# Performance work log

Hardware: AMD Instinct MI355X
Metric: run time of the kernel (lower is better)

The kernel has to match this reference:

```python
import jax, jax.numpy as jnp
import numpy as np

B, S, HID = 2, 2048, 2048
NH, HD, RD = 16, 128, 64
KVC, QC = 512, 1536


def _apply_rope(t):
    # t: [B, H, S, R]; standard half-split rotary embedding
    R = t.shape[-1]
    s = t.shape[-2]
    inv_freq = 1.0 / (10000.0 ** (jnp.arange(0, R, 2, dtype=jnp.float32) / R))  # [R/2]
    ang = jnp.arange(s, dtype=jnp.float32)[:, None] * inv_freq[None, :]  # [S, R/2]
    cos, sin = jnp.cos(ang), jnp.sin(ang)
    t1, t2 = t[..., : R // 2], t[..., R // 2 :]
    return jnp.concatenate([t1 * cos - t2 * sin, t2 * cos + t1 * sin], axis=-1)


def setup_inputs() -> dict:
    key = jax.random.key(0)
    ks = jax.random.split(key, 20)

    def lin(k, fan_in, fan_out):
        bound = 1.0 / np.sqrt(fan_in)
        kw, kb = jax.random.split(k)
        W = jax.random.uniform(kw, (fan_in, fan_out), jnp.float32, -bound, bound)
        b = jax.random.uniform(kb, (fan_out,), jnp.float32, -bound, bound)
        return W, b

    x = jax.random.normal(ks[0], (B, S, HID), jnp.float32)
    W_kvd, b_kvd = lin(ks[1], HID, KVC)
    W_ku, b_ku = lin(ks[2], KVC, NH * HD)
    W_vu, b_vu = lin(ks[3], KVC, NH * HD)
    W_kr, b_kr = lin(ks[4], KVC, NH * RD)
    W_qd, b_qd = lin(ks[5], HID, QC)
    W_qu, b_qu = lin(ks[6], QC, NH * HD)
    W_qr, b_qr = lin(ks[7], QC, NH * RD)
    W_o, b_o = lin(ks[8], NH * HD, HID)
    return dict(x=x, W_kvd=W_kvd, b_kvd=b_kvd, W_ku=W_ku, b_ku=b_ku,
                W_vu=W_vu, b_vu=b_vu, W_kr=W_kr, b_kr=b_kr,
                W_qd=W_qd, b_qd=b_qd, W_qu=W_qu, b_qu=b_qu,
                W_qr=W_qr, b_qr=b_qr, W_o=W_o, b_o=b_o)


def reference(x, W_kvd, b_kvd, W_ku, b_ku, W_vu, b_vu, W_kr, b_kr,
              W_qd, b_qd, W_qu, b_qu, W_qr, b_qr, W_o, b_o):
    b, s, _ = x.shape

    def heads(t, d):  # [B,S,NH*d] -> [B,NH,S,d]
        return t.reshape(b, s, NH, d).transpose(0, 2, 1, 3)

    kv_c = x @ W_kvd + b_kvd                     # [B,S,KVC]
    keys_c = heads(kv_c @ W_ku + b_ku, HD)       # [B,H,S,HD]
    values = heads(kv_c @ W_vu + b_vu, HD)
    keys_r = _apply_rope(heads(kv_c @ W_kr + b_kr, RD))

    q_c = x @ W_qd + b_qd                        # [B,S,QC]
    queries_c = heads(q_c @ W_qu + b_qu, HD)
    queries_r = _apply_rope(heads(q_c @ W_qr + b_qr, RD))

    q = jnp.concatenate([queries_c, queries_r], axis=-1)  # [B,H,S,HD+RD]
    k = jnp.concatenate([keys_c, keys_r], axis=-1)

    scale = 1.0 / np.sqrt(HD + RD)
    scores = jnp.einsum('bhqd,bhkd->bhqk', q, k) * scale
    causal = jnp.triu(jnp.ones((s, s), dtype=bool), k=1)
    scores = jnp.where(causal[None, None], jnp.float32(-1e9), scores)
    probs = jax.nn.softmax(scores, axis=-1)
    ctx = jnp.einsum('bhqk,bhkd->bhqd', probs, values)    # [B,H,S,HD]
    ctx = ctx.transpose(0, 2, 1, 3).reshape(b, s, NH * HD)
    return ctx @ W_o + b_o
```

## Files before the change

### kernel.cpp

```cpp
#include <hip/hip_runtime.h>
#include <math.h>

#define BB   2
#define SS   2048
#define HIDD 2048
#define NHH  16
#define HDD  128
#define RDD  64
#define KVCC 512
#define QCC  1536
#define DQK  192
#define MROWS 4096

using bf16x8 = __attribute__((ext_vector_type(8))) short;
using short4v = __attribute__((ext_vector_type(4))) short;
using f32x4  = __attribute__((ext_vector_type(4))) float;
using f32x16 = __attribute__((ext_vector_type(16))) float;

static __device__ __forceinline__ float b2f(short s) {
    unsigned u = ((unsigned)(unsigned short)s) << 16;
    union { unsigned u; float f; } v; v.u = u; return v.f;
}
static __device__ __forceinline__ short f2b(float f) {
    union { float f; unsigned u; } v; v.f = f;
    unsigned r = (v.u + 0x7fffu + ((v.u >> 16) & 1u)) >> 16;
    return (short)r;
}
static __device__ __forceinline__ unsigned cvtpk(float lo, float hi) {
    unsigned r;
    asm("v_cvt_pk_bf16_f32 %0, %1, %2" : "=v"(r) : "v"(lo), "v"(hi));
    return r;
}

#define GLOAD16(gsrc, ldst) \
    __builtin_amdgcn_global_load_lds((const __attribute__((address_space(1))) void*)(gsrc), \
                                     (__attribute__((address_space(3))) void*)(ldst), 16, 0, 0)

__global__ void prep_kernel(
    const float* __restrict__ W0, const float* __restrict__ W1,
    const float* __restrict__ W2, const float* __restrict__ W3,
    const float* __restrict__ W4, const float* __restrict__ W5,
    const float* __restrict__ W6, const float* __restrict__ W7,
    short* __restrict__ D0, short* __restrict__ D1,
    short* __restrict__ D2, short* __restrict__ D3,
    const float* __restrict__ x, short* __restrict__ xb,
    float2* __restrict__ tab) {
    __shared__ float t[32][33];
    int bid = blockIdx.x;
    int tx = threadIdx.x, ty = threadIdx.y;
    if (bid >= 17408) {
        int entry = (bid - 17408) * 256 + ty * 32 + tx;
        int s = entry >> 5, i = entry & 31;
        float inv = exp2f(-(float)i * 0.41524101186092034f);
        float sn, cs;
        sincosf((float)s * inv, &sn, &cs);
        tab[entry] = make_float2(cs, sn);
        return;
    }
    if (bid >= 15360) {
        int base = (bid - 15360) * 4096 + (ty * 32 + tx) * 16;
#pragma unroll
        for (int c = 0; c < 4; c++) {
            float4 v = *(const float4*)(x + base + c * 4);
            short4v o;
            o[0] = f2b(v.x); o[1] = f2b(v.y); o[2] = f2b(v.z); o[3] = f2b(v.w);
            *(short4v*)(xb + base + c * 4) = o;
        }
        return;
    }
    const float* W; short* Dst; int K, N, lt;
    if (bid < 4096) {
        if (bid < 1024) { W = W0; Dst = D0;                        K = 2048; N = 512;  lt = bid; }
        else            { W = W1; Dst = D0 + (size_t)512 * 2048;   K = 2048; N = 1536; lt = bid - 1024; }
    } else if (bid < 6656) {
        if (bid < 5120)      { W = W2; Dst = D1;                       K = 512; N = 2048; lt = bid - 4096; }
        else if (bid < 6144) { W = W3; Dst = D1 + (size_t)2048 * 512;  K = 512; N = 2048; lt = bid - 5120; }
        else                 { W = W4; Dst = D1 + (size_t)4096 * 512;  K = 512; N = 1024; lt = bid - 6144; }
    } else if (bid < 11264) {
        if (bid < 9728) { W = W5; Dst = D2;                        K = 1536; N = 2048; lt = bid - 6656; }
        else            { W = W6; Dst = D2 + (size_t)2048 * 1536;  K = 1536; N = 1024; lt = bid - 9728; }
    } else { W = W7; Dst = D3; K = 2048; N = 2048; lt = bid - 11264; }
    int ntx = N >> 5;
    int n0 = (lt % ntx) * 32, k0 = (lt / ntx) * 32;
#pragma unroll
    for (int i = 0; i < 4; i++)
        t[ty + i * 8][tx] = W[(size_t)(k0 + ty + i * 8) * N + n0 + tx];
    __syncthreads();
#pragma unroll
    for (int i = 0; i < 4; i++)
        Dst[(size_t)(n0 + ty + i * 8) * K + k0 + tx] = f2b(t[tx][ty + i * 8]);
}

template <int ID>
__global__ __launch_bounds__(256) void gemm128(
    const short* __restrict__ A, const short* __restrict__ Bt,
    const float* __restrict__ b0, const float* __restrict__ b1, const float* __restrict__ b2,
    void* __restrict__ C0, void* __restrict__ C1,
    const float2* __restrict__ tab,
    int M, int N, int K) {
    __shared__ short Asm[3][4096];
    __shared__ short Bsm[3][4096];
    int tid = threadIdx.x, lane = tid & 63, w = tid >> 6;
    int wm = w >> 1, wn = w & 1;
    int nbx = N >> 7;
    int cpx = gridDim.x >> 3;
    int swz = ((int)blockIdx.x & 7) * cpx + ((int)blockIdx.x >> 3);
    int m0 = (swz / nbx) * 128, n0 = (swz % nbx) * 128;
    int fr = lane & 15, fk = (lane >> 4) * 8;
    const short* Ag = A + (size_t)(m0 + (tid >> 2)) * K + (tid & 3) * 8;
    const short* Bg = Bt + (size_t)(n0 + (tid >> 2)) * K + (tid & 3) * 8;
    auto stage = [&](int t, int b) {
        int k0 = t * 32;
        GLOAD16(Ag + k0, &Asm[b][tid * 8]);
        GLOAD16(Ag + k0 + (size_t)64 * K, &Asm[b][2048 + tid * 8]);
        GLOAD16(Bg + k0, &Bsm[b][tid * 8]);
        GLOAD16(Bg + k0 + (size_t)64 * K, &Bsm[b][2048 + tid * 8]);
    };
    f32x4 acc[4][4] = {};
    int NT = K >> 5;
    stage(0, 0);
    stage(1, 1);
    for (int t = 0; t < NT; t++) {
        int cur = t % 3;
        if (t + 1 < NT) asm volatile("s_waitcnt vmcnt(4)" ::: "memory");
        else            asm volatile("s_waitcnt vmcnt(0)" ::: "memory");
        __builtin_amdgcn_s_barrier();
        bf16x8 af[4], bfv[4];
#pragma unroll
        for (int m = 0; m < 4; m++)
            af[m] = *(const bf16x8*)&Asm[cur][(wm * 64 + m * 16 + fr) * 32 + fk];
#pragma unroll
        for (int n = 0; n < 4; n++)
            bfv[n] = *(const bf16x8*)&Bsm[cur][(wn * 64 + n * 16 + fr) * 32 + fk];
#pragma unroll
        for (int m = 0; m < 4; m++)
#pragma unroll
            for (int n = 0; n < 4; n++)
                acc[m][n] = __builtin_amdgcn_mfma_f32_16x16x32_bf16(af[m], bfv[n], acc[m][n], 0, 0, 0);
        __builtin_amdgcn_s_barrier();
        if (t + 2 < NT) stage(t + 2, (t + 2) % 3);
    }
    bool ropeTile = (ID == 2 && n0 >= 4096) || (ID == 3 && n0 >= 2048);
    if (ropeTile) {
        int cbase = n0 - (ID == 2 ? 4096 : 2048) + wn * 64;
        int h = cbase >> 6;
        const float* bias = (ID == 2) ? b2 : b1;
        short* Dst = (short*)C0;
#pragma unroll
        for (int m = 0; m < 4; m++)
#pragma unroll
            for (int r = 0; r < 4; r++) {
                int row = m0 + wm * 64 + m * 16 + ((lane >> 4) << 2) + r;
                int b = row >> 11, s = row & (SS - 1);
                short* o = Dst + (((size_t)(b * NHH + h)) * SS + s) * DQK + HDD + (cbase & 63);
#pragma unroll
                for (int pp = 0; pp < 2; pp++) {
                    int i = pp * 16 + fr;
                    float2 cs = tab[s * 32 + i];
                    float vlo = acc[m][pp][r] + bias[cbase + pp * 16 + fr];
                    float vhi = acc[m][pp + 2][r] + bias[cbase + pp * 16 + 32 + fr];
                    o[i] = f2b(vlo * cs.x - vhi * cs.y);
                    o[i + 32] = f2b(vhi * cs.x + vlo * cs.y);
                }
            }
        return;
    }
#pragma unroll
    for (int m = 0; m < 4; m++)
#pragma unroll
        for (int n = 0; n < 4; n++)
#pragma unroll
            for (int r = 0; r < 4; r++) {
                int row = m0 + wm * 64 + m * 16 + ((lane >> 4) << 2) + r;
                int col = n0 + wn * 64 + n * 16 + fr;
                float v = acc[m][n][r];
                if constexpr (ID == 0) {
                    ((float*)C0)[(size_t)row * N + col] = v + b0[col];
                } else if constexpr (ID == 1) {
                    if (col < KVCC)
                        ((short*)C0)[(size_t)row * KVCC + col] = f2b(v + b0[col]);
                    else
                        ((short*)C1)[(size_t)row * QCC + (col - KVCC)] = f2b(v + b1[col - KVCC]);
                } else if constexpr (ID == 2) {
                    int b = row >> 11, s = row & (SS - 1);
                    if (col < 2048) {
                        int h = col >> 7, d = col & 127;
                        ((short*)C0)[(((size_t)(b * NHH + h)) * SS + s) * DQK + d] = f2b(v + b0[col]);
                    } else {
                        int c = col - 2048; int h = c >> 7, d = c & 127;
                        ((short*)C1)[(((size_t)(b * NHH + h)) * HDD + d) * SS + s] = f2b(v + b1[c]);
                    }
                } else {
                    int b = row >> 11, s = row & (SS - 1);
                    int h = col >> 7, d = col & 127;
                    ((short*)C0)[(((size_t)(b * NHH + h)) * SS + s) * DQK + d] = f2b(v + b0[col]);
                }
            }
}

__global__ __launch_bounds__(256, 2) void attn_kernel(
    const short* __restrict__ Q, const short* __restrict__ Kg,
    const short* __restrict__ Vt, short* __restrict__ ctx) {
    __shared__ short Ksm[2][64 * 192];
    __shared__ short Vsm[2][128 * 64];
    int tid = threadIdx.x, lane = tid & 63, w = tid >> 6;
    int hf = lane >> 5, l31 = lane & 31;
    int bid = blockIdx.x;
    int half = bid >> 8, a = (bid & 255) >> 5;
    int qt = half ? a : 15 - a;
    int bh = bid & 31;
    int bb = bh >> 4, hd = bh & 15;
    int q0 = qt * 128;
    const short* Qp = Q + (size_t)bh * SS * DQK;
    const short* Kp = Kg + (size_t)bh * SS * DQK;
    const char*  Vp = (const char*)(Vt + (size_t)bh * HDD * SS);
    int wr0 = q0 + w * 32;
    int qrow = wr0 + l31;
    const float scale = 0.07216878364870323f;
    const float L2E = 1.44269504088896f;

    bf16x8 qf[12];
#pragma unroll
    for (int s = 0; s < 12; s++)
        qf[s] = *(const bf16x8*)(Qp + (size_t)qrow * DQK + s * 16 + hf * 8);

    f32x16 acc[4] = {};
    float mrow = -1e30f, lsum = 0.f;
    int nt = 2 * qt + 2;

    auto stageK = [&](int key0, int b) {
#pragma unroll
        for (int pp = 0; pp < 6; pp++) {
            int flat = pp * 4096 + tid * 16;
            int row = flat / 384, bir = flat - row * 384;
            const char* src = (const char*)Kp + (size_t)(key0 + row) * 384 + (bir ^ ((row & 7) << 4));
            GLOAD16(src, (char*)Ksm[b] + flat);
        }
    };
    auto stageV = [&](int key0, int b) {
#pragma unroll
        for (int c = 0; c < 4; c++) {
            int flat = c * 4096 + tid * 16;
            int d = flat >> 7, bik = flat & 127;
            const char* src = Vp + (size_t)d * (SS * 2) + (size_t)key0 * 2 + (bik ^ ((d & 7) << 4));
            GLOAD16(src, (char*)Vsm[b] + flat);
        }
    };

    stageK(0, 0); stageV(0, 0);
    __syncthreads();

    for (int t0 = 0; t0 < nt; t0++) {
        int key0 = t0 * 64;
        int cur = t0 & 1;
        if (t0 + 1 < nt) { stageK(key0 + 64, cur ^ 1); stageV(key0 + 64, cur ^ 1); }
        bool active = (key0 <= wr0 + 31);
        if (active) {
            f32x16 z = {};
            f32x16 s0a = z, s0b = z, s1a = z, s1b = z;
            int xr = (l31 & 7) << 4;
            const char* Kb = (const char*)Ksm[cur];
            __builtin_amdgcn_s_setprio(1);
#pragma unroll
            for (int s = 0; s < 12; s += 2) {
                bf16x8 k0 = *(const bf16x8*)(Kb + l31 * 384 + ((s * 32 + hf * 16) ^ xr));
                bf16x8 k1 = *(const bf16x8*)(Kb + (32 + l31) * 384 + ((s * 32 + hf * 16) ^ xr));
                s0a = __builtin_amdgcn_mfma_f32_32x32x16_bf16(k0, qf[s], s0a, 0, 0, 0);
                s1a = __builtin_amdgcn_mfma_f32_32x32x16_bf16(k1, qf[s], s1a, 0, 0, 0);
                bf16x8 k0b = *(const bf16x8*)(Kb + l31 * 384 + (((s + 1) * 32 + hf * 16) ^ xr));
                bf16x8 k1b = *(const bf16x8*)(Kb + (32 + l31) * 384 + (((s + 1) * 32 + hf * 16) ^ xr));
                s0b = __builtin_amdgcn_mfma_f32_32x32x16_bf16(k0b, qf[s + 1], s0b, 0, 0, 0);
                s1b = __builtin_amdgcn_mfma_f32_32x32x16_bf16(k1b, qf[s + 1], s1b, 0, 0, 0);
            }
            __builtin_amdgcn_s_setprio(0);
            f32x16 sv0 = s0a + s0b, sv1 = s1a + s1b;
            bool domask = (key0 + 63 > wr0);
            float p[32];
#pragma unroll
            for (int t = 0; t < 2; t++)
#pragma unroll
                for (int r = 0; r < 16; r++) {
                    float v = (t ? sv1[r] : sv0[r]);
                    int key = key0 + 32 * t + (r & 3) + 8 * (r >> 2) + 4 * hf;
                    if (domask && key > qrow) v = -1e30f;
                    p[t * 16 + r] = v;
                }
            float tm[16];
#pragma unroll
            for (int i = 0; i < 16; i++) tm[i] = fmaxf(p[i], p[i + 16]);
#pragma unroll
            for (int i = 0; i < 8; i++) tm[i] = fmaxf(tm[i], tm[i + 8]);
#pragma unroll
            for (int i = 0; i < 4; i++) tm[i] = fmaxf(tm[i], tm[i + 4]);
            float pmaxs = fmaxf(fmaxf(tm[0], tm[1]), fmaxf(tm[2], tm[3])) * scale;
            if (__any(pmaxs > mrow + 8.f)) {
                float pc = fmaxf(pmaxs, __shfl_xor(pmaxs, 32, 64));
                float mn = fmaxf(mrow, pc);
                float al = exp2f((mrow - mn) * L2E);
                mrow = mn;
                lsum *= al;
                float arl[16];
#pragma unroll
                for (int r = 0; r < 16; r++)
                    arl[r] = __shfl(al, (r & 3) + 8 * (r >> 2) + 4 * hf, 64);
#pragma unroll
                for (int n = 0; n < 4; n++)
#pragma unroll
                    for (int r = 0; r < 16; r++)
                        acc[n][r] *= arl[r];
            }
            float sL = scale * L2E, mL = mrow * L2E;
#pragma unroll
            for (int i = 0; i < 32; i++)
                p[i] = exp2f(fmaf(p[i], sL, -mL));
            float ts[16];
#pragma unroll
            for (int i = 0; i < 16; i++) ts[i] = p[i] + p[i + 16];
#pragma unroll
            for (int i = 0; i < 8; i++) ts[i] = ts[i] + ts[i + 8];
#pragma unroll
            for (int i = 0; i < 4; i++) ts[i] = ts[i] + ts[i + 4];
            lsum += (ts[0] + ts[1]) + (ts[2] + ts[3]);
            bf16x8 afv[4];
#pragma unroll
            for (int g = 0; g < 4; g++) {
                int base = (g >> 1) * 16 + (g & 1) * 8;
                unsigned a01 = cvtpk(p[base + 0], p[base + 1]);
                unsigned a23 = cvtpk(p[base + 2], p[base + 3]);
                unsigned b01 = cvtpk(p[base + 4], p[base + 5]);
                unsigned b23 = cvtpk(p[base + 6], p[base + 7]);
                unsigned s0 = hf ? a01 : b01, s1 = hf ? a23 : b23;
                unsigned r0 = (unsigned)__shfl_xor((int)s0, 32, 64);
                unsigned r1 = (unsigned)__shfl_xor((int)s1, 32, 64);
                union { unsigned u[4]; bf16x8 v; } af;
                af.u[0] = hf ? r0 : a01;
                af.u[1] = hf ? r1 : a23;
                af.u[2] = hf ? b01 : r0;
                af.u[3] = hf ? b23 : r1;
                afv[g] = af.v;
            }
            const char* Vb = (const char*)Vsm[cur];
            __builtin_amdgcn_s_setprio(1);
#pragma unroll
            for (int g = 0; g < 4; g++)
#pragma unroll
                for (int n = 0; n < 4; n++) {
                    int d = n * 32 + l31;
                    bf16x8 vf = *(const bf16x8*)(Vb + d * 128 + ((g * 32 + hf * 16) ^ ((d & 7) << 4)));
                    acc[n] = __builtin_amdgcn_mfma_f32_32x32x16_bf16(afv[g], vf, acc[n], 0, 0, 0);
                }
            __builtin_amdgcn_s_setprio(0);
        }
        __syncthreads();
    }
    lsum += __shfl_xor(lsum, 32, 64);
    float rc = 1.0f / lsum;
    float rcl[16];
#pragma unroll
    for (int r = 0; r < 16; r++)
        rcl[r] = __shfl(rc, (r & 3) + 8 * (r >> 2) + 4 * hf, 64);
#pragma unroll
    for (int n = 0; n < 4; n++)
#pragma unroll
        for (int r = 0; r < 16; r++) {
            int row = wr0 + (r & 3) + 8 * (r >> 2) + 4 * hf;
            int d = n * 32 + l31;
            ctx[((size_t)(bb * SS + row)) * (NHH * HDD) + hd * HDD + d] = f2b(acc[n][r] * rcl[r]);
        }
}

extern "C" void kernel_launch(void* const* d_in, const int* in_sizes, int n_in,
                              void* d_out, int out_size, void* d_ws, size_t ws_size,
                              hipStream_t stream) {
    const float* x     = (const float*)d_in[0];
    const float* W_kvd = (const float*)d_in[1];  const float* b_kvd = (const float*)d_in[2];
    const float* W_ku  = (const float*)d_in[3];  const float* b_ku  = (const float*)d_in[4];
    const float* W_vu  = (const float*)d_in[5];  const float* b_vu  = (const float*)d_in[6];
    const float* W_kr  = (const float*)d_in[7];  const float* b_kr  = (const float*)d_in[8];
    const float* W_qd  = (const float*)d_in[9];  const float* b_qd  = (const float*)d_in[10];
    const float* W_qu  = (const float*)d_in[11]; const float* b_qu  = (const float*)d_in[12];
    const float* W_qr  = (const float*)d_in[13]; const float* b_qr  = (const float*)d_in[14];
    const float* W_o   = (const float*)d_in[15]; const float* b_o   = (const float*)d_in[16];
    float* out = (float*)d_out;

    char* p = (char*)d_ws;
    auto alloc = [&](size_t elems) {
        short* r = (short*)p;
        p += ((elems * 2) + 255) & ~(size_t)255;
        return r;
    };
    short* xb   = alloc((size_t)MROWS * HIDD);
    short* kvc  = alloc((size_t)MROWS * KVCC);
    short* qc   = alloc((size_t)MROWS * QCC);
    short* kbuf = alloc((size_t)BB * NHH * SS * DQK);
    short* qbuf = alloc((size_t)BB * NHH * SS * DQK);
    short* vtb  = alloc((size_t)BB * NHH * HDD * SS);
    short* ctx  = alloc((size_t)MROWS * NHH * HDD);
    short* Wt1  = alloc((size_t)2048 * 2048);
    short* Wt2  = alloc((size_t)5120 * 512);
    short* Wt3  = alloc((size_t)3072 * 1536);
    short* Wt4  = alloc((size_t)2048 * 2048);
    float2* tab = (float2*)alloc((size_t)65536 * 4);

    dim3 tb(32, 8);
    prep_kernel<<<dim3(17664), tb, 0, stream>>>(
        W_kvd, W_qd, W_ku, W_vu, W_kr, W_qu, W_qr, W_o, Wt1, Wt2, Wt3, Wt4,
        x, xb, tab);

    gemm128<1><<<dim3(512), 256, 0, stream>>>(
        xb, Wt1, b_kvd, b_qd, nullptr, kvc, qc, nullptr, MROWS, 2048, 2048);
    gemm128<2><<<dim3(1280), 256, 0, stream>>>(
        kvc, Wt2, b_ku, b_vu, b_kr, kbuf, vtb, tab, MROWS, 5120, 512);
    gemm128<3><<<dim3(768), 256, 0, stream>>>(
        qc, Wt3, b_qu, b_qr, nullptr, qbuf, nullptr, tab, MROWS, 3072, 1536);

    attn_kernel<<<dim3(512), 256, 0, stream>>>(qbuf, kbuf, vtb, ctx);

    gemm128<0><<<dim3(512), 256, 0, stream>>>(
        ctx, Wt4, b_o, nullptr, nullptr, out, nullptr, nullptr, MROWS, HIDD, NHH * HDD);
}
```

Measured before the change: 359.3 us.

## Software-pipeline QK of next tile with softmax/PV of current tile

Restructures the flash-attention key loop so the QK^T MFMAs for tile u are issued alongside the softmax and PV work for tile u-1. K and V staging are split into separately timed async loads, with fine-grained vmcnt waits and raw barriers replacing the full __syncthreads. The goal is to hide softmax latency behind matrix work and overlap the global-to-LDS loads. In exchange it holds more live score registers, and the correctness of the hand-written vmcnt counts depends on how many loads are in flight.

```diff
diff --git a/kernel.cpp b/kernel.cpp
--- a/kernel.cpp
+++ b/kernel.cpp
@@ -246,113 +246,138 @@
             GLOAD16(src, (char*)Vsm[b] + flat);
         }
     };
+    auto qk = [&](int u, const short* Kbuf, f32x16& o0, f32x16& o1) {
+        int key0 = u * 64;
+        if (key0 > wr0 + 31) return;
+        const char* Kb = (const char*)Kbuf;
+        f32x16 z = {};
+        f32x16 a0 = z, a1 = z;
+        int xr = (l31 & 7) << 4;
+        __builtin_amdgcn_s_setprio(1);
+#pragma unroll
+        for (int s = 0; s < 12; s++) {
+            bf16x8 k0 = *(const bf16x8*)(Kb + l31 * 384 + ((s * 32 + hf * 16) ^ xr));
+            bf16x8 k1 = *(const bf16x8*)(Kb + (32 + l31) * 384 + ((s * 32 + hf * 16) ^ xr));
+            a0 = __builtin_amdgcn_mfma_f32_32x32x16_bf16(k0, qf[s], a0, 0, 0, 0);
+            a1 = __builtin_amdgcn_mfma_f32_32x32x16_bf16(k1, qf[s], a1, 0, 0, 0);
+        }
+        __builtin_amdgcn_s_setprio(0);
+        o0 = a0; o1 = a1;
+    };
+    auto smpv = [&](int u, const f32x16& sv0, const f32x16& sv1, const short* Vbuf) {
+        int key0 = u * 64;
+        if (key0 > wr0 + 31) return;
+        bool domask = (key0 + 63 > wr0);
+        float p[32];
+#pragma unroll
+        for (int t = 0; t < 2; t++)
+#pragma unroll
+            for (int r = 0; r < 16; r++) {
+                float v = (t ? sv1[r] : sv0[r]);
+                int key = key0 + 32 * t + (r & 3) + 8 * (r >> 2) + 4 * hf;
+                if (domask && key > qrow) v = -1e30f;
+                p[t * 16 + r] = v;
+            }
+        float tm[16];
+#pragma unroll
+        for (int i = 0; i < 16; i++) tm[i] = fmaxf(p[i], p[i + 16]);
+#pragma unroll
+        for (int i = 0; i < 8; i++) tm[i] = fmaxf(tm[i], tm[i + 8]);
+#pragma unroll
+        for (int i = 0; i < 4; i++) tm[i] = fmaxf(tm[i], tm[i + 4]);
+        float pmaxs = fmaxf(fmaxf(tm[0], tm[1]), fmaxf(tm[2], tm[3])) * scale;
+        if (__any(pmaxs > mrow + 8.f)) {
+            float pc = fmaxf(pmaxs, __shfl_xor(pmaxs, 32, 64));
+            float mn = fmaxf(mrow, pc);
+            float al = exp2f((mrow - mn) * L2E);
+            mrow = mn;
+            lsum *= al;
+            float arl[16];
+#pragma unroll
+            for (int r = 0; r < 16; r++)
+                arl[r] = __shfl(al, (r & 3) + 8 * (r >> 2) + 4 * hf, 64);
+#pragma unroll
+            for (int n = 0; n < 4; n++)
+#pragma unroll
+                for (int r = 0; r < 16; r++)
+                    acc[n][r] *= arl[r];
+        }
+        float sL = scale * L2E, mL = mrow * L2E;
+#pragma unroll
+        for (int i = 0; i < 32; i++)
+            p[i] = exp2f(fmaf(p[i], sL, -mL));
+        float ts[16];
+#pragma unroll
+        for (int i = 0; i < 16; i++) ts[i] = p[i] + p[i + 16];
+#pragma unroll
+        for (int i = 0; i < 8; i++) ts[i] = ts[i] + ts[i + 8];
+#pragma unroll
+        for (int i = 0; i < 4; i++) ts[i] = ts[i] + ts[i + 4];
+        lsum += (ts[0] + ts[1]) + (ts[2] + ts[3]);
+        bf16x8 afv[4];
+#pragma unroll
+        for (int g = 0; g < 4; g++) {
+            int base = (g >> 1) * 16 + (g & 1) * 8;
+            unsigned a01 = cvtpk(p[base + 0], p[base + 1]);
+            unsigned a23 = cvtpk(p[base + 2], p[base + 3]);
+            unsigned b01 = cvtpk(p[base + 4], p[base + 5]);
+            unsigned b23 = cvtpk(p[base + 6], p[base + 7]);
+            unsigned s0 = hf ? a01 : b01, s1 = hf ? a23 : b23;
+            unsigned r0 = (unsigned)__shfl_xor((int)s0, 32, 64);
+            unsigned r1 = (unsigned)__shfl_xor((int)s1, 32, 64);
+            union { unsigned u[4]; bf16x8 v; } af;
+            af.u[0] = hf ? r0 : a01;
+            af.u[1] = hf ? r1 : a23;
+            af.u[2] = hf ? b01 : r0;
+            af.u[3] = hf ? b23 : r1;
+            afv[g] = af.v;
+        }
+        const char* Vb = (const char*)Vbuf;
+        __builtin_amdgcn_s_setprio(1);
+#pragma unroll
+        for (int g = 0; g < 4; g++)
+#pragma unroll
+            for (int n = 0; n < 4; n++) {
+                int d = n * 32 + l31;
+                bf16x8 vf = *(const bf16x8*)(Vb + d * 128 + ((g * 32 + hf * 16) ^ ((d & 7) << 4)));
+                acc[n] = __builtin_amdgcn_mfma_f32_32x32x16_bf16(afv[g], vf, acc[n], 0, 0, 0);
+            }
+        __builtin_amdgcn_s_setprio(0);
+    };
+
+    f32x16 svA0 = {}, svA1 = {}, svB0 = {}, svB1 = {};
 
     stageK(0, 0); stageV(0, 0);
-    __syncthreads();
-
-    for (int t0 = 0; t0 < nt; t0++) {
-        int key0 = t0 * 64;
-        int cur = t0 & 1;
-        if (t0 + 1 < nt) { stageK(key0 + 64, cur ^ 1); stageV(key0 + 64, cur ^ 1); }
-        bool active = (key0 <= wr0 + 31);
-        if (active) {
-            f32x16 z = {};
-            f32x16 s0a = z, s0b = z, s1a = z, s1b = z;
-            int xr = (l31 & 7) << 4;
-            const char* Kb = (const char*)Ksm[cur];
-            __builtin_amdgcn_s_setprio(1);
-#pragma unroll
-            for (int s = 0; s < 12; s += 2) {
-                bf16x8 k0 = *(const bf16x8*)(Kb + l31 * 384 + ((s * 32 + hf * 16) ^ xr));
-                bf16x8 k1 = *(const bf16x8*)(Kb + (32 + l31) * 384 + ((s * 32 + hf * 16) ^ xr));
-                s0a = __builtin_amdgcn_mfma_f32_32x32x16_bf16(k0, qf[s], s0a, 0, 0, 0);
-                s1a = __builtin_amdgcn_mfma_f32_32x32x16_bf16(k1, qf[s], s1a, 0, 0, 0);
-                bf16x8 k0b = *(const bf16x8*)(Kb + l31 * 384 + (((s + 1) * 32 + hf * 16) ^ xr));
-                bf16x8 k1b = *(const bf16x8*)(Kb + (32 + l31) * 384 + (((s + 1) * 32 + hf * 16) ^ xr));
-                s0b = __builtin_amdgcn_mfma_f32_32x32x16_bf16(k0b, qf[s + 1], s0b, 0, 0, 0);
-                s1b = __builtin_amdgcn_mfma_f32_32x32x16_bf16(k1b, qf[s + 1], s1b, 0, 0, 0);
-            }
-            __builtin_amdgcn_s_setprio(0);
-            f32x16 sv0 = s0a + s0b, sv1 = s1a + s1b;
-            bool domask = (key0 + 63 > wr0);
-            float p[32];
-#pragma unroll
-            for (int t = 0; t < 2; t++)
-#pragma unroll
-                for (int r = 0; r < 16; r++) {
-                    float v = (t ? sv1[r] : sv0[r]);
-                    int key = key0 + 32 * t + (r & 3) + 8 * (r >> 2) + 4 * hf;
-                    if (domask && key > qrow) v = -1e30f;
-                    p[t * 16 + r] = v;
-                }
-            float tm[16];
-#pragma unroll
-            for (int i = 0; i < 16; i++) tm[i] = fmaxf(p[i], p[i + 16]);
-#pragma unroll
-            for (int i = 0; i < 8; i++) tm[i] = fmaxf(tm[i], tm[i + 8]);
-#pragma unroll
-            for (int i = 0; i < 4; i++) tm[i] = fmaxf(tm[i], tm[i + 4]);
-            float pmaxs = fmaxf(fmaxf(tm[0], tm[1]), fmaxf(tm[2], tm[3])) * scale;
-            if (__any(pmaxs > mrow + 8.f)) {
-                float pc = fmaxf(pmaxs, __shfl_xor(pmaxs, 32, 64));
-                float mn = fmaxf(mrow, pc);
-                float al = exp2f((mrow - mn) * L2E);
-                mrow = mn;
-                lsum *= al;
-                float arl[16];
-#pragma unroll
-                for (int r = 0; r < 16; r++)
-                    arl[r] = __shfl(al, (r & 3) + 8 * (r >> 2) + 4 * hf, 64);
-#pragma unroll
-                for (int n = 0; n < 4; n++)
-#pragma unroll
-                    for (int r = 0; r < 16; r++)
-                        acc[n][r] *= arl[r];
-            }
-            float sL = scale * L2E, mL = mrow * L2E;
-#pragma unroll
-            for (int i = 0; i < 32; i++)
-                p[i] = exp2f(fmaf(p[i], sL, -mL));
-            float ts[16];
-#pragma unroll
-            for (int i = 0; i < 16; i++) ts[i] = p[i] + p[i + 16];
-#pragma unroll
-            for (int i = 0; i < 8; i++) ts[i] = ts[i] + ts[i + 8];
-#pragma unroll
-            for (int i = 0; i < 4; i++) ts[i] = ts[i] + ts[i + 4];
-            lsum += (ts[0] + ts[1]) + (ts[2] + ts[3]);
-            bf16x8 afv[4];
-#pragma unroll
-            for (int g = 0; g < 4; g++) {
-                int base = (g >> 1) * 16 + (g & 1) * 8;
-                unsigned a01 = cvtpk(p[base + 0], p[base + 1]);
-                unsigned a23 = cvtpk(p[base + 2], p[base + 3]);
-                unsigned b01 = cvtpk(p[base + 4], p[base + 5]);
-                unsigned b23 = cvtpk(p[base + 6], p[base + 7]);
-                unsigned s0 = hf ? a01 : b01, s1 = hf ? a23 : b23;
-                unsigned r0 = (unsigned)__shfl_xor((int)s0, 32, 64);
-                unsigned r1 = (unsigned)__shfl_xor((int)s1, 32, 64);
-                union { unsigned u[4]; bf16x8 v; } af;
-                af.u[0] = hf ? r0 : a01;
-                af.u[1] = hf ? r1 : a23;
-                af.u[2] = hf ? b01 : r0;
-                af.u[3] = hf ? b23 : r1;
-                afv[g] = af.v;
-            }
-            const char* Vb = (const char*)Vsm[cur];
-            __builtin_amdgcn_s_setprio(1);
-#pragma unroll
-            for (int g = 0; g < 4; g++)
-#pragma unroll
-                for (int n = 0; n < 4; n++) {
-                    int d = n * 32 + l31;
-                    bf16x8 vf = *(const bf16x8*)(Vb + d * 128 + ((g * 32 + hf * 16) ^ ((d & 7) << 4)));
-                    acc[n] = __builtin_amdgcn_mfma_f32_32x32x16_bf16(afv[g], vf, acc[n], 0, 0, 0);
-                }
-            __builtin_amdgcn_s_setprio(0);
-        }
-        __syncthreads();
+    asm volatile("s_waitcnt vmcnt(4)" ::: "memory");
+    __builtin_amdgcn_s_barrier();
+    stageK(64, 1);
+    qk(0, Ksm[0], svA0, svA1);
+    stageV(64, 1);
+
+    for (int u = 1; u + 1 < nt; u += 2) {
+        asm volatile("s_waitcnt vmcnt(4)" ::: "memory");
+        __builtin_amdgcn_s_barrier();
+        stageK((u + 1) * 64, 0);
+        qk(u, Ksm[1], svB0, svB1);
+        smpv(u - 1, svA0, svA1, Vsm[0]);
+        __builtin_amdgcn_s_barrier();
+        stageV((u + 1) * 64, 0);
+        asm volatile("s_waitcnt vmcnt(4)" ::: "memory");
+        __builtin_amdgcn_s_barrier();
+        if (u + 2 < nt) stageK((u + 2) * 64, 1);
+        qk(u + 1, Ksm[0], svA0, svA1);
+        smpv(u, svB0, svB1, Vsm[1]);
+        __builtin_amdgcn_s_barrier();
+        if (u + 2 < nt) stageV((u + 2) * 64, 1);
     }
+    asm volatile("s_waitcnt vmcnt(4)" ::: "memory");
+    __builtin_amdgcn_s_barrier();
+    qk(nt - 1, Ksm[1], svB0, svB1);
+    smpv(nt - 2, svA0, svA1, Vsm[0]);
+    asm volatile("s_waitcnt vmcnt(0)" ::: "memory");
+    __builtin_amdgcn_s_barrier();
+    smpv(nt - 1, svB0, svB1, Vsm[1]);
+
     lsum += __shfl_xor(lsum, 32, 64);
     float rc = 1.0f / lsum;
     float rcl[16];
```

Result: slower. 461.8 us (+28.5%).
